# Kernel tuning notes

Measured on AMD Instinct MI355X. Metric: run time of the kernel, lower is better.

The kernel has to match this reference:

```python
import jax, jax.numpy as jnp
import numpy as np

B, N, DIM = 8, 8192, 256
K, CDIM = 4096, 1024
COMMIT = 0.25


def setup_inputs() -> dict:
    key = jax.random.key(0)
    ks = jax.random.split(key, 4)
    x = jax.random.normal(ks[0], (B, N, DIM), dtype=jnp.float32)
    ln_g = jnp.ones((DIM,), jnp.float32)
    ln_b = jnp.zeros((DIM,), jnp.float32)
    w_pre = jax.random.normal(ks[1], (DIM, CDIM), jnp.float32) / np.sqrt(DIM)
    b_pre = jnp.zeros((CDIM,), jnp.float32)
    embed = jax.random.normal(ks[2], (K, CDIM), jnp.float32)
    w_post = jax.random.normal(ks[3], (CDIM, DIM), jnp.float32) / np.sqrt(CDIM)
    b_post = jnp.zeros((DIM,), jnp.float32)
    return {"x": x, "ln_g": ln_g, "ln_b": ln_b, "w_pre": w_pre, "b_pre": b_pre,
            "embed": embed, "w_post": w_post, "b_post": b_post}


def reference(x, ln_g, ln_b, w_pre, b_pre, embed, w_post, b_post):
    # LayerNorm over last dim (eps=1e-5, torch default)
    mu = jnp.mean(x, axis=-1, keepdims=True)
    var = jnp.mean((x - mu) ** 2, axis=-1, keepdims=True)
    xn = (x - mu) * jax.lax.rsqrt(var + 1e-5) * ln_g + ln_b
    # GELU (exact, erf-based as in torch default) then Linear dim->codebook_dim
    z_e = jax.nn.gelu(xn, approximate=False) @ w_pre + b_pre  # (B,N,CDIM)
    flat = z_e.reshape(-1, CDIM)                              # (B*N, CDIM)
    # squared euclidean distances to codebook, argmin, gather
    z_sq = jnp.sum(flat * flat, axis=1, keepdims=True)        # (BN,1)
    e_sq = jnp.sum(embed * embed, axis=1)                     # (K,)
    dist = z_sq - 2.0 * (flat @ embed.T) + e_sq[None, :]      # (BN,K)
    indices = jnp.argmin(dist, axis=1)                        # (BN,)
    z_q = embed[indices]                                      # (BN,CDIM)
    # commitment loss (z_q detached)
    commit = COMMIT * jnp.mean((flat - jax.lax.stop_gradient(z_q)) ** 2)
    # straight-through estimator
    z_q_st = flat + jax.lax.stop_gradient(z_q - flat)
    z_q_st = z_q_st.reshape(B, N, CDIM)
    quantized = z_q_st @ w_post + b_post                      # (B,N,DIM)
    return quantized, indices.reshape(B, N), commit
```

## Files before the change

### kernel.cpp

```cpp
#include <hip/hip_runtime.h>

#define BN_ROWS 65536
#define DIMX 256
#define CDIM 1024
#define KCODES 4096
#define NSP 16
#define NSLOT 5
#define NENT 6
#define CMARG 12.0f
#define RMARG 12.0f
#define QS 24.0f
#define INV_S2 (1.0f / (QS * QS))
#define FLT_BIG 3.402823466e+38f

static const size_t OFF_ESQ   = 0;
static const size_t OFF_IDXF  = 16384;
static const size_t OFF_CROW  = 278528;
static const size_t OFF_EPOST = 540672;
static const size_t OFF_EI8   = 4734976;
static const size_t OFF_NFLAG = 8929280;
static const size_t OFF_FLAG  = 8929344;
static const size_t OFF_CAND  = 9191488;

typedef __attribute__((ext_vector_type(4))) int i32x4;

#define GLOAD_LDS16(gsrc, ldst)                                                \
  __builtin_amdgcn_global_load_lds(                                            \
      (const __attribute__((address_space(1))) void*)(gsrc),                   \
      (__attribute__((address_space(3))) void*)(ldst), 16, 0, 0)

__device__ inline char q8(float f) {
  return (char)__float2int_rn(fminf(fmaxf(f * QS, -127.f), 127.f));
}
__device__ inline unsigned fkey(float s) {
  unsigned b = __float_as_uint(s);
  return b ^ ((unsigned)((int)b >> 31) | 0x80000000u);
}
__device__ inline float keyinv(unsigned k) {
  unsigned b = (k & 0x80000000u) ? (k ^ 0x80000000u) : ~k;
  return __uint_as_float(b);
}

__global__ __launch_bounds__(256) void k_esq(const float* __restrict__ embed,
                                             float* __restrict__ e_sq) {
  const int t = threadIdx.x, wv = t >> 6, lane = t & 63;
  const int row = blockIdx.x * 4 + wv;
  const float* e = embed + (size_t)row * CDIM;
  float s = 0.f;
  for (int k = lane * 4; k < CDIM; k += 256) {
    float4 v = *(const float4*)(e + k);
    s = fmaf(v.x, v.x, s); s = fmaf(v.y, v.y, s);
    s = fmaf(v.z, v.z, s); s = fmaf(v.w, v.w, s);
  }
#pragma unroll
  for (int o = 32; o > 0; o >>= 1) s += __shfl_xor(s, o);
  if (lane == 0) e_sq[row] = s;
}

__global__ __launch_bounds__(256) void k_ei8(const float* __restrict__ embed,
                                             char* __restrict__ Ei8) {
  const int t = threadIdx.x;
  const size_t row = blockIdx.x;
  float4 v = *(const float4*)(embed + row * CDIM + t * 4);
  *(char4*)(Ei8 + row * CDIM + t * 4) =
      make_char4(q8(v.x), q8(v.y), q8(v.z), q8(v.w));
}

__global__ __launch_bounds__(256) void k_ln_gelu_gemm(
    const float* __restrict__ x, const float* __restrict__ ln_g,
    const float* __restrict__ ln_b, const float* __restrict__ w_pre,
    const float* __restrict__ b_pre, float* __restrict__ zf,
    char* __restrict__ zi8, int row0) {
  __shared__ float g[16][DIMX];
  const int t = threadIdx.x;
  const int lrow0 = blockIdx.x * 16;
  const int grow0 = row0 + lrow0;
  const int wv = t >> 6, lane = t & 63;
#pragma unroll
  for (int j = 0; j < 4; ++j) {
    const int r = wv * 4 + j;
    const float* xr = x + (size_t)(grow0 + r) * DIMX;
    float4 v = *(const float4*)(xr + lane * 4);
    float s = v.x + v.y + v.z + v.w;
    float ss = v.x * v.x + v.y * v.y + v.z * v.z + v.w * v.w;
#pragma unroll
    for (int o = 32; o > 0; o >>= 1) { s += __shfl_xor(s, o); ss += __shfl_xor(ss, o); }
    const float mu = s * (1.0f / 256.0f);
    const float var = ss * (1.0f / 256.0f) - mu * mu;
    const float rstd = rsqrtf(var + 1e-5f);
    float vv[4] = {v.x, v.y, v.z, v.w};
#pragma unroll
    for (int q = 0; q < 4; ++q) {
      const int d = lane * 4 + q;
      float xn = (vv[q] - mu) * rstd * ln_g[d] + ln_b[d];
      g[r][d] = 0.5f * xn * (1.0f + erff(xn * 0.70710678118654752f));
    }
  }
  __syncthreads();
  float acc[16][4];
#pragma unroll
  for (int r = 0; r < 16; ++r)
#pragma unroll
    for (int c = 0; c < 4; ++c) acc[r][c] = 0.f;
#pragma unroll 2
  for (int d0 = 0; d0 < DIMX; d0 += 4) {
    float4 w0 = *(const float4*)(w_pre + (size_t)(d0 + 0) * CDIM + t * 4);
    float4 w1 = *(const float4*)(w_pre + (size_t)(d0 + 1) * CDIM + t * 4);
    float4 w2 = *(const float4*)(w_pre + (size_t)(d0 + 2) * CDIM + t * 4);
    float4 w3 = *(const float4*)(w_pre + (size_t)(d0 + 3) * CDIM + t * 4);
#pragma unroll
    for (int r = 0; r < 16; ++r) {
      float4 gv = *(const float4*)&g[r][d0];
      acc[r][0] = fmaf(gv.x, w0.x, acc[r][0]);
      acc[r][1] = fmaf(gv.x, w0.y, acc[r][1]);
      acc[r][2] = fmaf(gv.x, w0.z, acc[r][2]);
      acc[r][3] = fmaf(gv.x, w0.w, acc[r][3]);
      acc[r][0] = fmaf(gv.y, w1.x, acc[r][0]);
      acc[r][1] = fmaf(gv.y, w1.y, acc[r][1]);
      acc[r][2] = fmaf(gv.y, w1.z, acc[r][2]);
      acc[r][3] = fmaf(gv.y, w1.w, acc[r][3]);
      acc[r][0] = fmaf(gv.z, w2.x, acc[r][0]);
      acc[r][1] = fmaf(gv.z, w2.y, acc[r][1]);
      acc[r][2] = fmaf(gv.z, w2.z, acc[r][2]);
      acc[r][3] = fmaf(gv.z, w2.w, acc[r][3]);
      acc[r][0] = fmaf(gv.w, w3.x, acc[r][0]);
      acc[r][1] = fmaf(gv.w, w3.y, acc[r][1]);
      acc[r][2] = fmaf(gv.w, w3.z, acc[r][2]);
      acc[r][3] = fmaf(gv.w, w3.w, acc[r][3]);
    }
  }
  float4 bp = *(const float4*)(b_pre + t * 4);
#pragma unroll
  for (int r = 0; r < 16; ++r) {
    float4 o;
    o.x = acc[r][0] + bp.x; o.y = acc[r][1] + bp.y;
    o.z = acc[r][2] + bp.z; o.w = acc[r][3] + bp.w;
    *(float4*)(zf + (size_t)(lrow0 + r) * CDIM + t * 4) = o;
    *(char4*)(zi8 + (size_t)(lrow0 + r) * CDIM + t * 4) =
        make_char4(q8(o.x), q8(o.y), q8(o.z), q8(o.w));
  }
}

__global__ __launch_bounds__(512) void k_score(
    const char* __restrict__ Ei8, const char* __restrict__ Zi8,
    const float* __restrict__ e_sq, uint2* __restrict__ cand, int chunk) {
  __shared__ __align__(16) char lds[2][32768];
  const int t = threadIdx.x;
  const int cpx = gridDim.x >> 3;
  const int bx = (blockIdx.x & 7) * cpx + (blockIdx.x >> 3);
  const int zblk = bx / NSP, csp = bx % NSP;
  const int wid = t >> 6, l = t & 63;
  const int wr = wid >> 2, wc = wid & 3;
  const int lg = l >> 4, lo16 = l & 15;
  const int rowbase = zblk * 256;
  const int m0 = csp * 256;
  const int wr8 = wr * 8, wc4 = wc * 4, l16 = l * 16;

  const bool isA = (wid < 4);
  const int q = wid & 3;
  const char* sarr = isA ? Ei8 : Zi8;
  const int sbase = isA ? m0 : rowbase;
  const char* sp0 = sarr + (size_t)(sbase + q * 64 + lo16) * 1024 + lg * 16;
  const int dstbase = (isA ? 0 : 16384) + q * 4096;

  i32x4 acc[8][4];
#pragma unroll
  for (int mi = 0; mi < 8; ++mi)
#pragma unroll
    for (int ni = 0; ni < 4; ++ni) acc[mi][ni] = (i32x4){0, 0, 0, 0};

  {
    char* D = &lds[0][dstbase];
#pragma unroll
    for (int u = 0; u < 4; ++u) GLOAD_LDS16(sp0 + u * 16384, D + u * 1024);
  }

  for (int kt = 0; kt < 16; ++kt) {
    const char* Lc = lds[kt & 1];
    asm volatile("s_waitcnt vmcnt(0)" ::: "memory");
    __builtin_amdgcn_s_barrier();
    __builtin_amdgcn_sched_barrier(0);
    if (kt < 15) {
      char* Dst = &lds[(kt + 1) & 1][dstbase];
      const char* spk = sp0 + (kt + 1) * 64;
#pragma unroll
      for (int u = 0; u < 4; ++u) GLOAD_LDS16(spk + u * 16384, Dst + u * 1024);
    }
    i32x4 bh[4], a[8];
#pragma unroll
    for (int ni = 0; ni < 4; ++ni)
      bh[ni] = *(const i32x4*)(Lc + 16384 + (wc4 + ni) * 1024 + l16);
#pragma unroll
    for (int u = 0; u < 8; ++u)
      a[u] = *(const i32x4*)(Lc + (wr8 + u) * 1024 + l16);
    asm volatile("s_waitcnt lgkmcnt(0)" ::: "memory");
    __builtin_amdgcn_sched_barrier(0);
    __builtin_amdgcn_s_setprio(1);
#pragma unroll
    for (int u = 0; u < 8; ++u)
#pragma unroll
      for (int ni = 0; ni < 4; ++ni)
        acc[u][ni] = __builtin_amdgcn_mfma_i32_16x16x64_i8(a[u], bh[ni],
                                                           acc[u][ni], 0, 0, 0);
    __builtin_amdgcn_s_setprio(0);
  }

  float s1[4];
  int i1[4];
#pragma unroll
  for (int i = 0; i < 4; ++i) { s1[i] = FLT_BIG; i1[i] = 0x7fffffff; }
#pragma unroll
  for (int mi = 0; mi < 8; ++mi) {
    const int c0 = m0 + wr * 128 + mi * 16 + lg * 4;
    float4 es = *(const float4*)(e_sq + c0);
    float esv[4] = {es.x, es.y, es.z, es.w};
#pragma unroll
    for (int ni = 0; ni < 4; ++ni) {
#pragma unroll
      for (int j = 0; j < 4; ++j) {
        const float s = fmaf(-2.0f * INV_S2, (float)acc[mi][ni][j], esv[j]);
        const int c = c0 + j;
        if (s < s1[ni] || (s == s1[ni] && c < i1[ni])) { s1[ni] = s; i1[ni] = c; }
      }
    }
  }

  unsigned long long* red = (unsigned long long*)&lds[0][0];
  float* sb = (float*)&lds[0][4096];
  unsigned* sbi = (unsigned*)&lds[0][5120];
  unsigned* cnt = (unsigned*)&lds[0][6144];
  uint2* slot = (uint2*)&lds[0][7168];

  __syncthreads();
#pragma unroll
  for (int ni = 0; ni < 4; ++ni) {
    unsigned long long k1v =
        (((unsigned long long)fkey(s1[ni])) << 32) | (unsigned)i1[ni];
    unsigned long long o1 = __shfl_xor(k1v, 16);
    k1v = o1 < k1v ? o1 : k1v;
    o1 = __shfl_xor(k1v, 32);
    k1v = o1 < k1v ? o1 : k1v;
    if (lg == 0) {
      const int r = wc * 64 + ni * 16 + lo16;
      red[r * 2 + wr] = k1v;
    }
  }
  __syncthreads();
  if (t < 256) {
    unsigned long long a1 = red[t * 2 + 0], b1 = red[t * 2 + 1];
    if (b1 < a1) a1 = b1;
    sb[t] = keyinv((unsigned)(a1 >> 32));
    sbi[t] = (unsigned)(a1 & 0xFFFFFFFFull);
    cnt[t] = 0;
  }
  __syncthreads();
#pragma unroll
  for (int mi = 0; mi < 8; ++mi) {
    const int c0 = m0 + wr * 128 + mi * 16 + lg * 4;
    float4 es = *(const float4*)(e_sq + c0);
    float esv[4] = {es.x, es.y, es.z, es.w};
#pragma unroll
    for (int ni = 0; ni < 4; ++ni) {
      const int r = wc * 64 + ni * 16 + lo16;
      const float thr = sb[r] + CMARG;
#pragma unroll
      for (int j = 0; j < 4; ++j) {
        const float s = fmaf(-2.0f * INV_S2, (float)acc[mi][ni][j], esv[j]);
        const unsigned c = (unsigned)(c0 + j);
        if (s < thr && c != sbi[r]) {
          unsigned pos = atomicAdd(&cnt[r], 1u);
          if (pos < NSLOT)
            slot[r * NSLOT + pos] = make_uint2(__float_as_uint(s), c);
        }
      }
    }
  }
  __syncthreads();
  if (t < 256) {
    uint2* g = cand + (size_t)(rowbase + t) * (NSP * NENT) + csp * NENT;
    const unsigned ov = (cnt[t] > NSLOT) ? 0x40000000u : 0u;
    g[0] = make_uint2(__float_as_uint(sb[t]), sbi[t] | ov);
    const unsigned n = cnt[t] > NSLOT ? NSLOT : cnt[t];
#pragma unroll
    for (int k = 0; k < NSLOT; ++k)
      g[1 + k] = (k < (int)n) ? slot[t * NSLOT + k]
                              : make_uint2(__float_as_uint(FLT_BIG), 0xFFFFFFFFu);
  }
}

__global__ __launch_bounds__(256) void k_refine(
    const uint2* __restrict__ cand, const float* __restrict__ zf,
    const float* __restrict__ embed, int* __restrict__ idxf,
    float* __restrict__ crow, float* __restrict__ out_idx,
    int* __restrict__ flag_rows, int* __restrict__ nflag, int chunk,
    int row0) {
  const int t = threadIdx.x, wid = t >> 6, l = t & 63;
  const int lrow = blockIdx.x * 4 + wid;
  if (lrow >= chunk) return;
  const int grow = row0 + lrow;
  const uint2* base = cand + (size_t)lrow * (NSP * NENT);
  const uint2 e0 = base[l];
  const uint2 e1 = (l < 32) ? base[64 + l]
                            : make_uint2(__float_as_uint(FLT_BIG), 0xFFFFFFFFu);
  const bool is0 = (l % NENT) == 0;
  const bool is1 = (l < 32) && (((64 + l) % NENT) == 0);
  float gm = FLT_BIG;
  if (is0) gm = fminf(gm, __uint_as_float(e0.x));
  if (is1) gm = fminf(gm, __uint_as_float(e1.x));
#pragma unroll
  for (int o = 32; o > 0; o >>= 1) gm = fminf(gm, __shfl_xor(gm, o));
  const float thr = gm + RMARG;
  bool myovf = (is0 && (e0.y & 0x40000000u) && __uint_as_float(e0.x) < thr) ||
               (is1 && (e1.y & 0x40000000u) && __uint_as_float(e1.x) < thr);
  const bool ovf = __any(myovf);

  float zv[16];
#pragma unroll
  for (int j = 0; j < 16; ++j) zv[j] = zf[(size_t)lrow * CDIM + l + 64 * j];

  double d1 = 1e300;
  int i1 = 0x7fffffff;
#define PROC(E)                                                                \
  {                                                                            \
    const float sc_ = __uint_as_float(E.x);                                    \
    const int id_ = (int)(E.y & 0xFFFFu);                                      \
    unsigned long long mask = __ballot(sc_ < thr && id_ < KCODES);             \
    while (mask) {                                                             \
      const int src = __ffsll((unsigned long long)mask) - 1;                   \
      mask &= mask - 1;                                                        \
      const int c = __shfl(id_, src);                                          \
      const float* e = embed + (size_t)c * CDIM;                               \
      double dd = 0.0;                                                         \
      _Pragma("unroll") for (int j = 0; j < 16; ++j) {                         \
        const double df = (double)zv[j] - (double)e[l + 64 * j];               \
        dd = fma(df, df, dd);                                                  \
      }                                                                        \
      _Pragma("unroll") for (int o = 32; o > 0; o >>= 1) dd +=                 \
          __shfl_xor(dd, o);                                                   \
      if (dd < d1 || (dd == d1 && c < i1)) { d1 = dd; i1 = c; }                \
    }                                                                          \
  }
  PROC(e0);
  PROC(e1);
#undef PROC
  if (l == 0) {
    idxf[grow] = i1;
    out_idx[grow] = (float)i1;
    crow[grow] = (float)d1;
    if (ovf) {
      const int s = atomicAdd(nflag, 1);
      flag_rows[s] = lrow;
    }
  }
}

__global__ __launch_bounds__(256) void k_exact(
    const float* __restrict__ zf, const float* __restrict__ embed,
    const int* __restrict__ flag_rows, const int* __restrict__ nflag,
    int* __restrict__ idxf, float* __restrict__ crow,
    float* __restrict__ out_idx, int row0) {
  __shared__ double wd[4];
  __shared__ int wcidx[4];
  const int t = threadIdx.x;
  const int wid = t >> 6, l = t & 63;
  const int n = *nflag;

  for (int fi = blockIdx.x; fi < n; fi += gridDim.x) {
    const int lrow = flag_rows[fi];
    const int grow = row0 + lrow;
    float zr[16];
#pragma unroll
    for (int j = 0; j < 16; ++j) zr[j] = zf[(size_t)lrow * CDIM + l + 64 * j];
    double dmin = 1e300;
    int cmin = 0x7fffffff;
    for (int ci = 0; ci < 1024; ++ci) {
      const int c = wid * 1024 + ci;
      const float* e = embed + (size_t)c * CDIM;
      double dd = 0.0;
#pragma unroll
      for (int j = 0; j < 16; ++j) {
        const double df = (double)zr[j] - (double)e[l + 64 * j];
        dd = fma(df, df, dd);
      }
#pragma unroll
      for (int o = 32; o > 0; o >>= 1) dd += __shfl_xor(dd, o);
      if (dd < dmin) { dmin = dd; cmin = c; }
    }
    if (l == 0) { wd[wid] = dmin; wcidx[wid] = cmin; }
    __syncthreads();
    if (t == 0) {
      double dm = wd[0]; int cm = wcidx[0];
#pragma unroll
      for (int wv = 1; wv < 4; ++wv) {
        if (wd[wv] < dm || (wd[wv] == dm && wcidx[wv] < cm)) {
          dm = wd[wv]; cm = wcidx[wv];
        }
      }
      idxf[grow] = cm;
      out_idx[grow] = (float)cm;
      crow[grow] = (float)dm;
    }
    __syncthreads();
  }
}

__global__ __launch_bounds__(256) void k_epost(const float* __restrict__ E,
                                               const float* __restrict__ w_post,
                                               float* __restrict__ E_post) {
  __shared__ float es[16][128];
  const int t = threadIdx.x;
  const int r0 = blockIdx.x * 16;
  float acc[16];
#pragma unroll
  for (int r = 0; r < 16; ++r) acc[r] = 0.f;
  for (int k0 = 0; k0 < CDIM; k0 += 128) {
    __syncthreads();
#pragma unroll
    for (int p = 0; p < 2; ++p) {
      const int fl = (p * 256 + t) * 4;
      const int r = fl >> 7, kk = fl & 127;
      float4 v = *(const float4*)(E + (size_t)(r0 + r) * CDIM + k0 + kk);
      *(float4*)&es[r][kk] = v;
    }
    __syncthreads();
#pragma unroll 4
    for (int d = 0; d < 128; ++d) {
      const float w = w_post[(size_t)(k0 + d) * DIMX + t];
#pragma unroll
      for (int r = 0; r < 16; ++r) acc[r] = fmaf(es[r][d], w, acc[r]);
    }
  }
#pragma unroll
  for (int r = 0; r < 16; ++r)
    E_post[(size_t)(r0 + r) * DIMX + t] = acc[r];
}

__global__ __launch_bounds__(256) void k_gather(const float* __restrict__ E_post,
                                                const int* __restrict__ idx,
                                                const float* __restrict__ b_post,
                                                float* __restrict__ outq) {
  const int t = threadIdx.x;
  const int r0 = blockIdx.x * 16;
  const float bp = b_post[t];
#pragma unroll
  for (int i = 0; i < 16; ++i) {
    const int row = r0 + i;
    outq[(size_t)row * DIMX + t] = E_post[(size_t)idx[row] * DIMX + t] + bp;
  }
}

__global__ __launch_bounds__(256) void k_commit_final(
    const float* __restrict__ crow, float* __restrict__ out_commit) {
  const int t = threadIdx.x;
  double s = 0.0;
  for (int i = t; i < BN_ROWS; i += 256) s += (double)crow[i];
#pragma unroll
  for (int o = 32; o > 0; o >>= 1) s += __shfl_xor(s, o);
  __shared__ double wsum[4];
  if ((t & 63) == 0) wsum[t >> 6] = s;
  __syncthreads();
  if (t == 0)
    *out_commit = (float)(0.25 * (wsum[0] + wsum[1] + wsum[2] + wsum[3]) /
                          (65536.0 * 1024.0));
}

extern "C" void kernel_launch(void* const* d_in, const int* in_sizes, int n_in,
                              void* d_out, int out_size, void* d_ws,
                              size_t ws_size, hipStream_t stream) {
  const float* x = (const float*)d_in[0];
  const float* ln_g = (const float*)d_in[1];
  const float* ln_b = (const float*)d_in[2];
  const float* w_pre = (const float*)d_in[3];
  const float* b_pre = (const float*)d_in[4];
  const float* embed = (const float*)d_in[5];
  const float* w_post = (const float*)d_in[6];
  const float* b_post = (const float*)d_in[7];

  float* out = (float*)d_out;
  float* outq = out;
  float* out_idx = out + 16777216;
  float* out_commit = out + 16842752;

  char* ws = (char*)d_ws;
  float* e_sq = (float*)(ws + OFF_ESQ);
  int* idxf = (int*)(ws + OFF_IDXF);
  float* crow = (float*)(ws + OFF_CROW);
  float* E_post = (float*)(ws + OFF_EPOST);
  char* Ei8 = (char*)(ws + OFF_EI8);
  int* nflag = (int*)(ws + OFF_NFLAG);
  int* flag_rows = (int*)(ws + OFF_FLAG);

  int chunk = 4096;
  while (chunk < BN_ROWS &&
         OFF_CAND + (size_t)(chunk * 2) * 5888ull <= ws_size)
    chunk *= 2;
  uint2* cand = (uint2*)(ws + OFF_CAND);
  char* zi8 = ws + OFF_CAND + (size_t)chunk * 768;
  float* zf = (float*)(ws + OFF_CAND + (size_t)chunk * 768 +
                       (size_t)chunk * 1024);

  k_esq<<<KCODES / 4, 256, 0, stream>>>(embed, e_sq);
  k_ei8<<<KCODES, 256, 0, stream>>>(embed, Ei8);
  k_epost<<<KCODES / 16, 256, 0, stream>>>(embed, w_post, E_post);

  for (int row0 = 0; row0 < BN_ROWS; row0 += chunk) {
    hipMemsetAsync(nflag, 0, sizeof(int), stream);
    k_ln_gelu_gemm<<<chunk / 16, 256, 0, stream>>>(x, ln_g, ln_b, w_pre, b_pre,
                                                   zf, zi8, row0);
    k_score<<<(chunk / 256) * NSP, 512, 0, stream>>>(Ei8, zi8, e_sq, cand,
                                                     chunk);
    k_refine<<<chunk / 4, 256, 0, stream>>>(cand, zf, embed, idxf, crow,
                                            out_idx, flag_rows, nflag, chunk,
                                            row0);
    k_exact<<<128, 256, 0, stream>>>(zf, embed, flag_rows, nflag, idxf, crow,
                                     out_idx, row0);
  }

  k_gather<<<BN_ROWS / 16, 256, 0, stream>>>(E_post, idxf, b_post, outq);
  k_commit_final<<<1, 256, 0, stream>>>(crow, out_commit);
}
```

Before: 1.331 ms.

## Fuse codebook prep kernels, enlarge LN-GEMM row tile, widen refine blocks

Merges the e_sq and int8-quantize codebook kernels into one pass over embed, so the codebook is read once instead of twice. Doubles the rows per block in the LN+GELU+GEMM kernel from 16 to 32, so each w_pre load is reused across more rows, and adds a launch-bounds occupancy hint. The refine kernel moves to 512-thread blocks handling 8 rows each. The larger accumulator tile (128 floats per thread) raises register pressure and could cause spills or lower occupancy.

```diff
diff --git a/kernel.cpp b/kernel.cpp
--- a/kernel.cpp
+++ b/kernel.cpp
@@ -12,6 +12,7 @@
 #define QS 24.0f
 #define INV_S2 (1.0f / (QS * QS))
 #define FLT_BIG 3.402823466e+38f
+#define K1ROWS 32
 
 static const size_t OFF_ESQ   = 0;
 static const size_t OFF_IDXF  = 16384;
@@ -41,44 +42,36 @@
   return __uint_as_float(b);
 }
 
-__global__ __launch_bounds__(256) void k_esq(const float* __restrict__ embed,
-                                             float* __restrict__ e_sq) {
+__global__ __launch_bounds__(256) void k_prep_e(const float* __restrict__ embed,
+                                                float* __restrict__ e_sq,
+                                                char* __restrict__ Ei8) {
   const int t = threadIdx.x, wv = t >> 6, lane = t & 63;
-  const int row = blockIdx.x * 4 + wv;
-  const float* e = embed + (size_t)row * CDIM;
-  float s = 0.f;
-  for (int k = lane * 4; k < CDIM; k += 256) {
-    float4 v = *(const float4*)(e + k);
-    s = fmaf(v.x, v.x, s); s = fmaf(v.y, v.y, s);
-    s = fmaf(v.z, v.z, s); s = fmaf(v.w, v.w, s);
-  }
-#pragma unroll
-  for (int o = 32; o > 0; o >>= 1) s += __shfl_xor(s, o);
-  if (lane == 0) e_sq[row] = s;
-}
-
-__global__ __launch_bounds__(256) void k_ei8(const float* __restrict__ embed,
-                                             char* __restrict__ Ei8) {
-  const int t = threadIdx.x;
   const size_t row = blockIdx.x;
   float4 v = *(const float4*)(embed + row * CDIM + t * 4);
   *(char4*)(Ei8 + row * CDIM + t * 4) =
       make_char4(q8(v.x), q8(v.y), q8(v.z), q8(v.w));
-}
-
-__global__ __launch_bounds__(256) void k_ln_gelu_gemm(
+  float s = v.x * v.x + v.y * v.y + v.z * v.z + v.w * v.w;
+#pragma unroll
+  for (int o = 32; o > 0; o >>= 1) s += __shfl_xor(s, o);
+  __shared__ float wsum[4];
+  if (lane == 0) wsum[wv] = s;
+  __syncthreads();
+  if (t == 0) e_sq[row] = wsum[0] + wsum[1] + wsum[2] + wsum[3];
+}
+
+__global__ __launch_bounds__(256, 2) void k_ln_gelu_gemm(
     const float* __restrict__ x, const float* __restrict__ ln_g,
     const float* __restrict__ ln_b, const float* __restrict__ w_pre,
     const float* __restrict__ b_pre, float* __restrict__ zf,
     char* __restrict__ zi8, int row0) {
-  __shared__ float g[16][DIMX];
+  __shared__ float g[K1ROWS][DIMX];
   const int t = threadIdx.x;
-  const int lrow0 = blockIdx.x * 16;
+  const int lrow0 = blockIdx.x * K1ROWS;
   const int grow0 = row0 + lrow0;
   const int wv = t >> 6, lane = t & 63;
 #pragma unroll
-  for (int j = 0; j < 4; ++j) {
-    const int r = wv * 4 + j;
+  for (int j = 0; j < 8; ++j) {
+    const int r = wv * 8 + j;
     const float* xr = x + (size_t)(grow0 + r) * DIMX;
     float4 v = *(const float4*)(xr + lane * 4);
     float s = v.x + v.y + v.z + v.w;
@@ -97,19 +90,18 @@
     }
   }
   __syncthreads();
-  float acc[16][4];
-#pragma unroll
-  for (int r = 0; r < 16; ++r)
+  float acc[K1ROWS][4];
+#pragma unroll
+  for (int r = 0; r < K1ROWS; ++r)
 #pragma unroll
     for (int c = 0; c < 4; ++c) acc[r][c] = 0.f;
-#pragma unroll 2
   for (int d0 = 0; d0 < DIMX; d0 += 4) {
     float4 w0 = *(const float4*)(w_pre + (size_t)(d0 + 0) * CDIM + t * 4);
     float4 w1 = *(const float4*)(w_pre + (size_t)(d0 + 1) * CDIM + t * 4);
     float4 w2 = *(const float4*)(w_pre + (size_t)(d0 + 2) * CDIM + t * 4);
     float4 w3 = *(const float4*)(w_pre + (size_t)(d0 + 3) * CDIM + t * 4);
 #pragma unroll
-    for (int r = 0; r < 16; ++r) {
+    for (int r = 0; r < K1ROWS; ++r) {
       float4 gv = *(const float4*)&g[r][d0];
       acc[r][0] = fmaf(gv.x, w0.x, acc[r][0]);
       acc[r][1] = fmaf(gv.x, w0.y, acc[r][1]);
@@ -131,7 +123,7 @@
   }
   float4 bp = *(const float4*)(b_pre + t * 4);
 #pragma unroll
-  for (int r = 0; r < 16; ++r) {
+  for (int r = 0; r < K1ROWS; ++r) {
     float4 o;
     o.x = acc[r][0] + bp.x; o.y = acc[r][1] + bp.y;
     o.z = acc[r][2] + bp.z; o.w = acc[r][3] + bp.w;
@@ -288,14 +280,14 @@
   }
 }
 
-__global__ __launch_bounds__(256) void k_refine(
+__global__ __launch_bounds__(512) void k_refine(
     const uint2* __restrict__ cand, const float* __restrict__ zf,
     const float* __restrict__ embed, int* __restrict__ idxf,
     float* __restrict__ crow, float* __restrict__ out_idx,
     int* __restrict__ flag_rows, int* __restrict__ nflag, int chunk,
     int row0) {
   const int t = threadIdx.x, wid = t >> 6, l = t & 63;
-  const int lrow = blockIdx.x * 4 + wid;
+  const int lrow = blockIdx.x * 8 + wid;
   if (lrow >= chunk) return;
   const int grow = row0 + lrow;
   const uint2* base = cand + (size_t)lrow * (NSP * NENT);
@@ -499,17 +491,16 @@
   float* zf = (float*)(ws + OFF_CAND + (size_t)chunk * 768 +
                        (size_t)chunk * 1024);
 
-  k_esq<<<KCODES / 4, 256, 0, stream>>>(embed, e_sq);
-  k_ei8<<<KCODES, 256, 0, stream>>>(embed, Ei8);
+  k_prep_e<<<KCODES, 256, 0, stream>>>(embed, e_sq, Ei8);
   k_epost<<<KCODES / 16, 256, 0, stream>>>(embed, w_post, E_post);
 
   for (int row0 = 0; row0 < BN_ROWS; row0 += chunk) {
     hipMemsetAsync(nflag, 0, sizeof(int), stream);
-    k_ln_gelu_gemm<<<chunk / 16, 256, 0, stream>>>(x, ln_g, ln_b, w_pre, b_pre,
-                                                   zf, zi8, row0);
+    k_ln_gelu_gemm<<<chunk / K1ROWS, 256, 0, stream>>>(x, ln_g, ln_b, w_pre,
+                                                       b_pre, zf, zi8, row0);
     k_score<<<(chunk / 256) * NSP, 512, 0, stream>>>(Ei8, zi8, e_sq, cand,
                                                      chunk);
-    k_refine<<<chunk / 4, 256, 0, stream>>>(cand, zf, embed, idxf, crow,
+    k_refine<<<chunk / 8, 512, 0, stream>>>(cand, zf, embed, idxf, crow,
                                             out_idx, flag_rows, nflag, chunk,
                                             row0);
     k_exact<<<128, 256, 0, stream>>>(zf, embed, flag_rows, nflag, idxf, crow,
```

Result: slower. 1.429 ms (+7.3%).
